# Performance work log

Hardware: AMD Instinct MI355X
Metric: run time of the kernel (lower is better)

Reference implementation:

```python
import jax, jax.numpy as jnp
import numpy as np

B, T, D, E, H, F, K = 4, 2048, 2048, 16, 1024, 1024, 2


def setup_inputs() -> dict:
    key = jax.random.key(0)
    ks = jax.random.split(key, 7)
    sD, sH, sF = D ** -0.5, H ** -0.5, F ** -0.5
    hidden_state = jax.random.normal(ks[0], (B, T, D), jnp.float32)
    Wr = jax.random.normal(ks[1], (D, E), jnp.float32) * sD      # router
    Wg = jax.random.normal(ks[2], (D, 1), jnp.float32) * sD      # shared gate
    W1 = jax.random.normal(ks[3], (E, D, H), jnp.float32) * sD   # expert up-proj
    W2 = jax.random.normal(ks[4], (E, H, D), jnp.float32) * sH   # expert down-proj
    W1s = jax.random.normal(ks[5], (D, F), jnp.float32) * sD     # shared expert up
    W2s = jax.random.normal(ks[6], (F, D), jnp.float32) * sF     # shared expert down
    return {"hidden_state": hidden_state, "Wr": Wr, "Wg": Wg,
            "W1": W1, "W2": W2, "W1s": W1s, "W2s": W2s}


def reference(hidden_state, Wr, Wg, W1, W2, W1s, W2s):
    b, t, d = hidden_state.shape
    N = b * t
    x = hidden_state.reshape(N, d)

    # Router: softmax scores + shared-expert sigmoid gate
    s = jax.nn.softmax(x @ Wr, axis=-1)           # [N, E]
    g_shared = jax.nn.sigmoid(x @ Wg)             # [N, 1]

    topk_vals, topk_idx = jax.lax.top_k(s, K)     # [N, K]

    # Dense combine weights: gate[n,e] = topk_vals if expert e chosen, else 0.
    # Mathematically identical to sort/gather/scatter-add dispatch in the source.
    gate = jnp.zeros((N, E), dtype=s.dtype).at[
        jnp.arange(N)[:, None], topk_idx].add(topk_vals)

    # Per-expert FFN (fixed small expert loop), gate-weighted combine
    y = jnp.zeros_like(x)
    for e in range(E):
        h = jax.nn.gelu(x @ W1[e], approximate=False)   # [N, H]
        y = y + gate[:, e:e + 1] * (h @ W2[e])

    # Shared expert, scaled by sigmoid gate
    shared = jax.nn.gelu(x @ W1s, approximate=False) @ W2s
    y = y + g_shared * shared
    y_out = y.reshape(b, t, d)

    # Aux stats (attention_mask is None branch)
    importance = s.mean(axis=0)                               # [E]
    counts = jnp.zeros((E,), jnp.float32).at[topk_idx.reshape(-1)].add(1.0)
    load = counts / (counts.sum() + 1e-12)
    return y_out, importance, load
```

## Files before the change

### kernel.cpp

```cpp
#include <hip/hip_runtime.h>
#include <hip/hip_bf16.h>


#define N_TOK 8192
#define DDIM  2048
#define NEXP  16
#define HDIM  1024
#define FDIM  1024
#define NASSIGN (N_TOK * 2)
#define NROWS (NASSIGN + N_TOK)

typedef __attribute__((ext_vector_type(8))) short bf16x8;
typedef __attribute__((ext_vector_type(4))) float f32x4;
typedef __attribute__((ext_vector_type(8))) unsigned short u16x8;
typedef __attribute__((ext_vector_type(4))) unsigned short u16x4;

__device__ inline unsigned short f2bf(float f) {
    unsigned int u = __builtin_bit_cast(unsigned int, f);
    u += 0x7FFFu + ((u >> 16) & 1u);
    return (unsigned short)(u >> 16);
}

__device__ inline float bf2f(unsigned short h) {
    return __builtin_bit_cast(float, (unsigned int)h << 16);
}

__device__ inline float gelu_f(float v) {
    return 0.5f * v * (1.0f + erff(v * 0.7071067811865475f));
}

__device__ inline void gld16(void* lds, const void* g) {
    __builtin_amdgcn_global_load_lds(
        (const __attribute__((address_space(1))) unsigned int*)g,
        (__attribute__((address_space(3))) unsigned int*)lds, 16, 0, 0);
}

__global__ __launch_bounds__(256) void zero_small(float* imp) {
    if (threadIdx.x < NEXP) imp[threadIdx.x] = 0.0f;
}

__global__ __launch_bounds__(256) void cast_x_kernel(const float* __restrict__ x,
                                                     unsigned short* __restrict__ xb) {
    size_t i = (size_t)blockIdx.x * 256 + threadIdx.x;
    const float4 a = ((const float4*)x)[i * 2];
    const float4 b = ((const float4*)x)[i * 2 + 1];
    u16x8 o;
    o[0] = f2bf(a.x); o[1] = f2bf(a.y); o[2] = f2bf(a.z); o[3] = f2bf(a.w);
    o[4] = f2bf(b.x); o[5] = f2bf(b.y); o[6] = f2bf(b.z); o[7] = f2bf(b.w);
    *(u16x8*)(xb + i * 8) = o;
}

template <int R, int C>
__global__ __launch_bounds__(256) void transpose_cast(const float* __restrict__ src,
                                                      unsigned short* __restrict__ dst) {
    __shared__ unsigned short t[64][66];
    const size_t zoff = (size_t)blockIdx.z * R * C;
    src += zoff; dst += zoff;
    const int r0 = blockIdx.y * 64, c0 = blockIdx.x * 64;
    const int tid = threadIdx.x;
    const int cr = tid >> 4;
    const int cc4 = (tid & 15) * 4;
#pragma unroll
    for (int it = 0; it < 4; ++it) {
        int row = cr + it * 16;
        const float4 v = *(const float4*)(src + (size_t)(r0 + row) * C + c0 + cc4);
        t[row][cc4 + 0] = f2bf(v.x); t[row][cc4 + 1] = f2bf(v.y);
        t[row][cc4 + 2] = f2bf(v.z); t[row][cc4 + 3] = f2bf(v.w);
    }
    __syncthreads();
#pragma unroll
    for (int it = 0; it < 4; ++it) {
        int cc = cr + it * 16;
        u16x4 o;
#pragma unroll
        for (int j = 0; j < 4; ++j) o[j] = t[cc4 + j][cc];
        *(u16x4*)(dst + (size_t)(c0 + cc) * R + r0 + cc4) = o;
    }
}

__global__ __launch_bounds__(256) void router_kernel(
    const float* __restrict__ x, const float* __restrict__ Wr, const float* __restrict__ Wg,
    float* __restrict__ gsh, int* __restrict__ t2i, float* __restrict__ t2v,
    float* __restrict__ imp) {
    __shared__ float simp[NEXP];
    const int tid = threadIdx.x, lane = tid & 63, w = tid >> 6;
    if (tid < NEXP) simp[tid] = 0.0f;
    __syncthreads();
    const int n = blockIdx.x * 4 + w;
    const float* xr = x + (size_t)n * DDIM;
    float acc[NEXP];
#pragma unroll
    for (int e = 0; e < NEXP; ++e) acc[e] = 0.0f;
    float ag = 0.0f;
    for (int j = 0; j < DDIM / 64; ++j) {
        int d = lane + j * 64;
        float xv = xr[d];
        const float* wr = Wr + (size_t)d * NEXP;
#pragma unroll
        for (int e = 0; e < NEXP; ++e) acc[e] = fmaf(xv, wr[e], acc[e]);
        ag = fmaf(xv, Wg[d], ag);
    }
#pragma unroll
    for (int off = 32; off; off >>= 1) {
#pragma unroll
        for (int e = 0; e < NEXP; ++e) acc[e] += __shfl_xor(acc[e], off);
        ag += __shfl_xor(ag, off);
    }
    if (lane == 0) {
        float mx = acc[0];
#pragma unroll
        for (int e = 1; e < NEXP; ++e) mx = fmaxf(mx, acc[e]);
        float p[NEXP], s = 0.0f;
#pragma unroll
        for (int e = 0; e < NEXP; ++e) { p[e] = expf(acc[e] - mx); s += p[e]; }
        const float inv = 1.0f / s;
        int i1 = 0; float v1 = -1.0f;
#pragma unroll
        for (int e = 0; e < NEXP; ++e) {
            p[e] *= inv;
            if (p[e] > v1) { v1 = p[e]; i1 = e; }
        }
        int i2 = 0; float v2 = -1.0f;
#pragma unroll
        for (int e = 0; e < NEXP; ++e) {
            if (e != i1 && p[e] > v2) { v2 = p[e]; i2 = e; }
        }
        t2i[2 * n] = i1; t2i[2 * n + 1] = i2;
        t2v[2 * n] = v1; t2v[2 * n + 1] = v2;
        gsh[n] = 1.0f / (1.0f + expf(-ag));
#pragma unroll
        for (int e = 0; e < NEXP; ++e) atomicAdd(&simp[e], p[e]);
    }
    __syncthreads();
    if (tid < NEXP) unsafeAtomicAdd(&imp[tid], simp[tid]);
}

__global__ __launch_bounds__(256) void scan_finalize(
    const int* __restrict__ t2i, const float* __restrict__ imp,
    int* __restrict__ offs, int* __restrict__ fill, float* __restrict__ out_tail) {
    __shared__ int hist[NEXP];
    const int tid = threadIdx.x;
    if (tid < NEXP) hist[tid] = 0;
    __syncthreads();
    for (int i = tid; i < NASSIGN; i += 256) atomicAdd(&hist[t2i[i]], 1);
    __syncthreads();
    if (tid == 0) {
        int o = 0;
        for (int e = 0; e < NEXP; ++e) { offs[e] = o; o += hist[e]; }
        offs[NEXP] = o;
        offs[NEXP + 1] = NROWS;
    }
    if (tid < NEXP) {
        fill[tid] = 0;
        out_tail[tid] = imp[tid] * (1.0f / (float)N_TOK);
        out_tail[NEXP + tid] = (float)hist[tid] / (float)NASSIGN;
    }
}

__global__ __launch_bounds__(256) void build_assign(
    const int* __restrict__ t2i, const float* __restrict__ t2v,
    const int* __restrict__ offs, int* __restrict__ fill,
    const float* __restrict__ gsh,
    int* __restrict__ atok, float* __restrict__ agate, int* __restrict__ t2pos) {
    const int n = blockIdx.x * 256 + threadIdx.x;
#pragma unroll
    for (int k = 0; k < 2; ++k) {
        int e = t2i[2 * n + k];
        int pos = offs[e] + atomicAdd(&fill[e], 1);
        atok[pos] = n;
        agate[pos] = t2v[2 * n + k];
        t2pos[2 * n + k] = pos;
    }
    atok[NASSIGN + n] = n;
    agate[NASSIGN + n] = gsh[n];
}

__global__ __launch_bounds__(256) void combine_kernel(
    const unsigned short* __restrict__ contrib, const int* __restrict__ t2pos,
    float* __restrict__ y) {
    const int gi = blockIdx.x * 256 + threadIdx.x;
    const int n = gi >> 8;
    const int d8 = (gi & 255) * 8;
    const int p0 = t2pos[2 * n], p1 = t2pos[2 * n + 1];
    u16x8 a = *(const u16x8*)(contrib + (size_t)p0 * DDIM + d8);
    u16x8 b = *(const u16x8*)(contrib + (size_t)p1 * DDIM + d8);
    u16x8 c = *(const u16x8*)(contrib + (size_t)(NASSIGN + n) * DDIM + d8);
    float4 y0, y1;
    y0.x = bf2f(a[0]) + bf2f(b[0]) + bf2f(c[0]);
    y0.y = bf2f(a[1]) + bf2f(b[1]) + bf2f(c[1]);
    y0.z = bf2f(a[2]) + bf2f(b[2]) + bf2f(c[2]);
    y0.w = bf2f(a[3]) + bf2f(b[3]) + bf2f(c[3]);
    y1.x = bf2f(a[4]) + bf2f(b[4]) + bf2f(c[4]);
    y1.y = bf2f(a[5]) + bf2f(b[5]) + bf2f(c[5]);
    y1.z = bf2f(a[6]) + bf2f(b[6]) + bf2f(c[6]);
    y1.w = bf2f(a[7]) + bf2f(b[7]) + bf2f(c[7]);
    float* yr = y + (size_t)n * DDIM + d8;
    *(float4*)yr = y0;
    *(float4*)(yr + 4) = y1;
}

template <int MODE>
__global__ __launch_bounds__(256, 4) void gemm128(
    const unsigned short* __restrict__ A, const unsigned short* __restrict__ B,
    unsigned short* __restrict__ out,
    const int* __restrict__ offs, const int* __restrict__ atok,
    const float* __restrict__ agate) {
    constexpr int KD = MODE == 0 ? DDIM : HDIM;
    constexpr int NC = MODE == 0 ? HDIM : DDIM;
    const int e = blockIdx.z;
    const int m0 = offs[e];
    const int mE = offs[e + 1] - m0;
    const int tm = blockIdx.y;
    if (tm * 128 >= mE) return;
    const int n0 = blockIdx.x * 128;

    __shared__ __align__(16) unsigned short As_[2][128 * 32];
    __shared__ __align__(16) unsigned short Bs_[2][128 * 32];

    const int tid = threadIdx.x, lane = tid & 63;
    const int wid = tid >> 6, wm = wid >> 1, wn = wid & 1;

    const unsigned short* sA[2];
    const unsigned short* sB[2];
    int dOff[2];
#pragma unroll
    for (int it = 0; it < 2; ++it) {
        int c = tid + it * 256;
        int row = c >> 2, slot = c & 3;
        int ksw = (slot ^ ((row >> 1) & 3)) * 8;
        int arow = tm * 128 + row; arow = arow < mE ? arow : mE - 1;
        if (MODE == 0)
            sA[it] = A + (size_t)atok[m0 + arow] * KD + ksw;
        else
            sA[it] = A + (size_t)(m0 + arow) * KD + ksw;
        sB[it] = B + (size_t)e * KD * NC + (size_t)(n0 + row) * KD + ksw;
        dOff[it] = c * 16;
    }

    f32x4 acc[4][4] = {};

    auto stage = [&](int b, int kk) {
        gld16((char*)As_[b] + dOff[0], sA[0] + kk);
        gld16((char*)As_[b] + dOff[1], sA[1] + kk);
        gld16((char*)Bs_[b] + dOff[0], sB[0] + kk);
        gld16((char*)Bs_[b] + dOff[1], sB[1] + kk);
    };
    auto compute = [&](int b) {
        const int c16 = lane & 15, q = lane >> 4;
        bf16x8 av[4], bv[4];
#pragma unroll
        for (int mi = 0; mi < 4; ++mi) {
            int r = wm * 64 + mi * 16 + c16;
            int s = q ^ ((r >> 1) & 3);
            av[mi] = *(const bf16x8*)((const char*)As_[b] + r * 64 + s * 16);
        }
#pragma unroll
        for (int ni = 0; ni < 4; ++ni) {
            int r = wn * 64 + ni * 16 + c16;
            int s = q ^ ((r >> 1) & 3);
            bv[ni] = *(const bf16x8*)((const char*)Bs_[b] + r * 64 + s * 16);
        }
#pragma unroll
        for (int mi = 0; mi < 4; ++mi)
#pragma unroll
            for (int ni = 0; ni < 4; ++ni)
                acc[mi][ni] = __builtin_amdgcn_mfma_f32_16x16x32_bf16(
                    av[mi], bv[ni], acc[mi][ni], 0, 0, 0);
    };

    stage(0, 0);
    __syncthreads();

#pragma unroll 1
    for (int kk = 0; kk < KD; kk += 64) {
        stage(1, kk + 32);
        compute(0);
        __syncthreads();
        if (kk + 64 < KD) stage(0, kk + 64);
        compute(1);
        __syncthreads();
    }

    const int col = lane & 15, r4 = (lane >> 4) * 4;
#pragma unroll
    for (int mi = 0; mi < 4; ++mi) {
#pragma unroll
        for (int r = 0; r < 4; ++r) {
            int grow = tm * 128 + wm * 64 + mi * 16 + r4 + r;
            if (grow >= mE) continue;
            float gate = (MODE == 0) ? agate[m0 + grow] : 0.0f;
#pragma unroll
            for (int ni = 0; ni < 4; ++ni) {
                int gcol = n0 + wn * 64 + ni * 16 + col;
                float v = acc[mi][ni][r];
                if (MODE == 0)
                    out[(size_t)(m0 + grow) * NC + gcol] = f2bf(gelu_f(v) * gate);
                else
                    out[(size_t)(m0 + grow) * NC + gcol] = f2bf(v);
            }
        }
    }
}

extern "C" void kernel_launch(void* const* d_in, const int* in_sizes, int n_in,
                              void* d_out, int out_size, void* d_ws, size_t ws_size,
                              hipStream_t stream) {
    const float* x   = (const float*)d_in[0];
    const float* Wr  = (const float*)d_in[1];
    const float* Wg  = (const float*)d_in[2];
    const float* W1  = (const float*)d_in[3];
    const float* W2  = (const float*)d_in[4];
    const float* W1s = (const float*)d_in[5];
    const float* W2s = (const float*)d_in[6];
    float* out = (float*)d_out;

    char* ws = (char*)d_ws;
    size_t off = 0;
    auto carve = [&](size_t bytes) { char* p = ws + off; off += (bytes + 255) & ~(size_t)255; return p; };
    unsigned short* xb    = (unsigned short*)carve((size_t)N_TOK * DDIM * 2);
    unsigned short* w1all = (unsigned short*)carve((size_t)(NEXP + 1) * DDIM * HDIM * 2);
    unsigned short* w2all = (unsigned short*)carve((size_t)(NEXP + 1) * HDIM * DDIM * 2);
    unsigned short* hb    = (unsigned short*)carve((size_t)NROWS * HDIM * 2);
    float* gsh            = (float*)carve((size_t)N_TOK * 4);
    int* t2i              = (int*)carve((size_t)N_TOK * 2 * 4);
    float* t2v            = (float*)carve((size_t)N_TOK * 2 * 4);
    int* atok             = (int*)carve((size_t)NROWS * 4);
    float* agate          = (float*)carve((size_t)NROWS * 4);
    int* t2pos            = (int*)carve((size_t)NASSIGN * 4);
    float* imp            = (float*)carve(256);
    int* offs             = (int*)carve(256);
    int* fill             = (int*)carve(256);
    if (ws_size < off) return;

    unsigned short* contrib = (unsigned short*)ws;

    float* out_tail = out + (size_t)N_TOK * DDIM;

    hipLaunchKernelGGL(zero_small, dim3(1), dim3(256), 0, stream, imp);
    hipLaunchKernelGGL(cast_x_kernel, dim3(N_TOK * DDIM / 8 / 256), dim3(256), 0, stream, x, xb);
    hipLaunchKernelGGL((transpose_cast<DDIM, HDIM>), dim3(HDIM / 64, DDIM / 64, NEXP), dim3(256), 0, stream, W1, w1all);
    hipLaunchKernelGGL((transpose_cast<DDIM, HDIM>), dim3(HDIM / 64, DDIM / 64, 1), dim3(256), 0, stream,
                       W1s, w1all + (size_t)NEXP * DDIM * HDIM);
    hipLaunchKernelGGL((transpose_cast<HDIM, DDIM>), dim3(DDIM / 64, HDIM / 64, NEXP), dim3(256), 0, stream, W2, w2all);
    hipLaunchKernelGGL((transpose_cast<HDIM, DDIM>), dim3(DDIM / 64, HDIM / 64, 1), dim3(256), 0, stream,
                       W2s, w2all + (size_t)NEXP * HDIM * DDIM);
    hipLaunchKernelGGL(router_kernel, dim3(N_TOK / 4), dim3(256), 0, stream, x, Wr, Wg, gsh, t2i, t2v, imp);
    hipLaunchKernelGGL(scan_finalize, dim3(1), dim3(256), 0, stream, t2i, imp, offs, fill, out_tail);
    hipLaunchKernelGGL(build_assign, dim3(N_TOK / 256), dim3(256), 0, stream, t2i, t2v, offs, fill, gsh, atok, agate, t2pos);

    hipLaunchKernelGGL((gemm128<0>), dim3(HDIM / 128, N_TOK / 128, NEXP + 1), dim3(256), 0, stream,
                       xb, w1all, hb, offs, atok, agate);
    hipLaunchKernelGGL((gemm128<1>), dim3(DDIM / 128, N_TOK / 128, NEXP + 1), dim3(256), 0, stream,
                       hb, w2all, contrib, offs, atok, agate);
    hipLaunchKernelGGL(combine_kernel, dim3(N_TOK * DDIM / 8 / 256), dim3(256), 0, stream,
                       contrib, t2pos, out);
}
```

Before: 614.6 us.

## Fuse bf16 cast of x into router and swizzle grouped GEMM block order

The standalone cast_x kernel is removed and the bf16 conversion of x is written from the router kernel, which already reads x. This saves one full pass over the fp32 activations and one launch. The grouped GEMMs now use a flattened 1D grid with an XCD-style modulo-8 remap of block indices to 3D coordinates, so that blocks sharing tiles land on the same chiplet L2. The router's bf16 stores are 2-byte strided per lane, so they coalesce less well than the old vectorized cast.

```diff
diff --git a/kernel.cpp b/kernel.cpp
--- a/kernel.cpp
+++ b/kernel.cpp
@@ -37,17 +37,6 @@
 
 __global__ __launch_bounds__(256) void zero_small(float* imp) {
     if (threadIdx.x < NEXP) imp[threadIdx.x] = 0.0f;
-}
-
-__global__ __launch_bounds__(256) void cast_x_kernel(const float* __restrict__ x,
-                                                     unsigned short* __restrict__ xb) {
-    size_t i = (size_t)blockIdx.x * 256 + threadIdx.x;
-    const float4 a = ((const float4*)x)[i * 2];
-    const float4 b = ((const float4*)x)[i * 2 + 1];
-    u16x8 o;
-    o[0] = f2bf(a.x); o[1] = f2bf(a.y); o[2] = f2bf(a.z); o[3] = f2bf(a.w);
-    o[4] = f2bf(b.x); o[5] = f2bf(b.y); o[6] = f2bf(b.z); o[7] = f2bf(b.w);
-    *(u16x8*)(xb + i * 8) = o;
 }
 
 template <int R, int C>
@@ -80,6 +69,7 @@
 
 __global__ __launch_bounds__(256) void router_kernel(
     const float* __restrict__ x, const float* __restrict__ Wr, const float* __restrict__ Wg,
+    unsigned short* __restrict__ xb,
     float* __restrict__ gsh, int* __restrict__ t2i, float* __restrict__ t2v,
     float* __restrict__ imp) {
     __shared__ float simp[NEXP];
@@ -88,6 +78,7 @@
     __syncthreads();
     const int n = blockIdx.x * 4 + w;
     const float* xr = x + (size_t)n * DDIM;
+    unsigned short* xbr = xb + (size_t)n * DDIM;
     float acc[NEXP];
 #pragma unroll
     for (int e = 0; e < NEXP; ++e) acc[e] = 0.0f;
@@ -95,6 +86,7 @@
     for (int j = 0; j < DDIM / 64; ++j) {
         int d = lane + j * 64;
         float xv = xr[d];
+        xbr[d] = f2bf(xv);
         const float* wr = Wr + (size_t)d * NEXP;
 #pragma unroll
         for (int e = 0; e < NEXP; ++e) acc[e] = fmaf(xv, wr[e], acc[e]);
@@ -207,12 +199,22 @@
     const float* __restrict__ agate) {
     constexpr int KD = MODE == 0 ? DDIM : HDIM;
     constexpr int NC = MODE == 0 ? HDIM : DDIM;
-    const int e = blockIdx.z;
+    constexpr int NX = NC / 128;
+    constexpr int NY = N_TOK / 128;
+    constexpr int NZ = NEXP + 1;
+    constexpr int NB = NX * NY * NZ;
+    static_assert(NB % 8 == 0, "bijective swizzle needs NB % 8 == 0");
+
+    const int L = blockIdx.x;
+    const int orig = (L & 7) * (NB / 8) + (L >> 3);
+    const int bx = orig % NX;
+    const int tm = (orig / NX) % NY;
+    const int e  = orig / (NX * NY);
+
     const int m0 = offs[e];
     const int mE = offs[e + 1] - m0;
-    const int tm = blockIdx.y;
     if (tm * 128 >= mE) return;
-    const int n0 = blockIdx.x * 128;
+    const int n0 = bx * 128;
 
     __shared__ __align__(16) unsigned short As_[2][128 * 32];
     __shared__ __align__(16) unsigned short Bs_[2][128 * 32];
@@ -337,20 +339,19 @@
     float* out_tail = out + (size_t)N_TOK * DDIM;
 
     hipLaunchKernelGGL(zero_small, dim3(1), dim3(256), 0, stream, imp);
-    hipLaunchKernelGGL(cast_x_kernel, dim3(N_TOK * DDIM / 8 / 256), dim3(256), 0, stream, x, xb);
     hipLaunchKernelGGL((transpose_cast<DDIM, HDIM>), dim3(HDIM / 64, DDIM / 64, NEXP), dim3(256), 0, stream, W1, w1all);
     hipLaunchKernelGGL((transpose_cast<DDIM, HDIM>), dim3(HDIM / 64, DDIM / 64, 1), dim3(256), 0, stream,
                        W1s, w1all + (size_t)NEXP * DDIM * HDIM);
     hipLaunchKernelGGL((transpose_cast<HDIM, DDIM>), dim3(DDIM / 64, HDIM / 64, NEXP), dim3(256), 0, stream, W2, w2all);
     hipLaunchKernelGGL((transpose_cast<HDIM, DDIM>), dim3(DDIM / 64, HDIM / 64, 1), dim3(256), 0, stream,
                        W2s, w2all + (size_t)NEXP * HDIM * DDIM);
-    hipLaunchKernelGGL(router_kernel, dim3(N_TOK / 4), dim3(256), 0, stream, x, Wr, Wg, gsh, t2i, t2v, imp);
+    hipLaunchKernelGGL(router_kernel, dim3(N_TOK / 4), dim3(256), 0, stream, x, Wr, Wg, xb, gsh, t2i, t2v, imp);
     hipLaunchKernelGGL(scan_finalize, dim3(1), dim3(256), 0, stream, t2i, imp, offs, fill, out_tail);
     hipLaunchKernelGGL(build_assign, dim3(N_TOK / 256), dim3(256), 0, stream, t2i, t2v, offs, fill, gsh, atok, agate, t2pos);
 
-    hipLaunchKernelGGL((gemm128<0>), dim3(HDIM / 128, N_TOK / 128, NEXP + 1), dim3(256), 0, stream,
+    hipLaunchKernelGGL((gemm128<0>), dim3((HDIM / 128) * (N_TOK / 128) * (NEXP + 1)), dim3(256), 0, stream,
                        xb, w1all, hb, offs, atok, agate);
-    hipLaunchKernelGGL((gemm128<1>), dim3(DDIM / 128, N_TOK / 128, NEXP + 1), dim3(256), 0, stream,
+    hipLaunchKernelGGL((gemm128<1>), dim3((DDIM / 128) * (N_TOK / 128) * (NEXP + 1)), dim3(256), 0, stream,
                        hb, w2all, contrib, offs, atok, agate);
     hipLaunchKernelGGL(combine_kernel, dim3(N_TOK * DDIM / 8 / 256), dim3(256), 0, stream,
                        contrib, t2pos, out);
```

Result: slower. 966.5 us (+57.2%).

## Triple-buffer GEMM LDS pipeline and fuse x bf16 cast into router

Applied to the files above, without the earlier changes.

The grouped GEMM moves from a double-buffered K loop with two __syncthreads per 64-wide step to a three-stage LDS ring. Each tile step now needs one barrier, and explicit vmcnt waits keep a prefetch in flight while computing. Separately, the standalone x→bf16 cast kernel is removed and the router writes xb as it reads x, saving one full pass over x and a launch. The extra LDS buffer lowers the occupancy bound from 4 to 3 blocks per SM, and the router's 2-byte per-lane stores are narrow.

```diff
diff --git a/kernel.cpp b/kernel.cpp
--- a/kernel.cpp
+++ b/kernel.cpp
@@ -37,17 +37,6 @@
 
 __global__ __launch_bounds__(256) void zero_small(float* imp) {
     if (threadIdx.x < NEXP) imp[threadIdx.x] = 0.0f;
-}
-
-__global__ __launch_bounds__(256) void cast_x_kernel(const float* __restrict__ x,
-                                                     unsigned short* __restrict__ xb) {
-    size_t i = (size_t)blockIdx.x * 256 + threadIdx.x;
-    const float4 a = ((const float4*)x)[i * 2];
-    const float4 b = ((const float4*)x)[i * 2 + 1];
-    u16x8 o;
-    o[0] = f2bf(a.x); o[1] = f2bf(a.y); o[2] = f2bf(a.z); o[3] = f2bf(a.w);
-    o[4] = f2bf(b.x); o[5] = f2bf(b.y); o[6] = f2bf(b.z); o[7] = f2bf(b.w);
-    *(u16x8*)(xb + i * 8) = o;
 }
 
 template <int R, int C>
@@ -80,6 +69,7 @@
 
 __global__ __launch_bounds__(256) void router_kernel(
     const float* __restrict__ x, const float* __restrict__ Wr, const float* __restrict__ Wg,
+    unsigned short* __restrict__ xb,
     float* __restrict__ gsh, int* __restrict__ t2i, float* __restrict__ t2v,
     float* __restrict__ imp) {
     __shared__ float simp[NEXP];
@@ -88,6 +78,7 @@
     __syncthreads();
     const int n = blockIdx.x * 4 + w;
     const float* xr = x + (size_t)n * DDIM;
+    unsigned short* xbr = xb + (size_t)n * DDIM;
     float acc[NEXP];
 #pragma unroll
     for (int e = 0; e < NEXP; ++e) acc[e] = 0.0f;
@@ -95,6 +86,7 @@
     for (int j = 0; j < DDIM / 64; ++j) {
         int d = lane + j * 64;
         float xv = xr[d];
+        xbr[d] = f2bf(xv);
         const float* wr = Wr + (size_t)d * NEXP;
 #pragma unroll
         for (int e = 0; e < NEXP; ++e) acc[e] = fmaf(xv, wr[e], acc[e]);
@@ -200,13 +192,14 @@
 }
 
 template <int MODE>
-__global__ __launch_bounds__(256, 4) void gemm128(
+__global__ __launch_bounds__(256, 3) void gemm128(
     const unsigned short* __restrict__ A, const unsigned short* __restrict__ B,
     unsigned short* __restrict__ out,
     const int* __restrict__ offs, const int* __restrict__ atok,
     const float* __restrict__ agate) {
     constexpr int KD = MODE == 0 ? DDIM : HDIM;
     constexpr int NC = MODE == 0 ? HDIM : DDIM;
+    constexpr int NT = KD / 32;
     const int e = blockIdx.z;
     const int m0 = offs[e];
     const int mE = offs[e + 1] - m0;
@@ -214,8 +207,8 @@
     if (tm * 128 >= mE) return;
     const int n0 = blockIdx.x * 128;
 
-    __shared__ __align__(16) unsigned short As_[2][128 * 32];
-    __shared__ __align__(16) unsigned short Bs_[2][128 * 32];
+    __shared__ __align__(16) unsigned short As_[3][128 * 32];
+    __shared__ __align__(16) unsigned short Bs_[3][128 * 32];
 
     const int tid = threadIdx.x, lane = tid & 63;
     const int wid = tid >> 6, wm = wid >> 1, wn = wid & 1;
@@ -239,7 +232,8 @@
 
     f32x4 acc[4][4] = {};
 
-    auto stage = [&](int b, int kk) {
+    auto stage = [&](int b, int t) {
+        const int kk = t * 32;
         gld16((char*)As_[b] + dOff[0], sA[0] + kk);
         gld16((char*)As_[b] + dOff[1], sA[1] + kk);
         gld16((char*)Bs_[b] + dOff[0], sB[0] + kk);
@@ -269,16 +263,33 @@
     };
 
     stage(0, 0);
-    __syncthreads();
-
+    stage(1, 1);
+    asm volatile("s_waitcnt vmcnt(4)" ::: "memory");
+    __builtin_amdgcn_sched_barrier(0);
+    __builtin_amdgcn_s_barrier();
+    __builtin_amdgcn_sched_barrier(0);
+
+    int b = 0, bn = 2;
 #pragma unroll 1
-    for (int kk = 0; kk < KD; kk += 64) {
-        stage(1, kk + 32);
-        compute(0);
-        __syncthreads();
-        if (kk + 64 < KD) stage(0, kk + 64);
-        compute(1);
-        __syncthreads();
+    for (int t = 0; t < NT; ++t) {
+        if (t + 2 < NT) {
+            stage(bn, t + 2);
+            compute(b);
+            asm volatile("s_waitcnt vmcnt(4)" ::: "memory");
+            __builtin_amdgcn_sched_barrier(0);
+            __builtin_amdgcn_s_barrier();
+            __builtin_amdgcn_sched_barrier(0);
+        } else if (t + 1 < NT) {
+            compute(b);
+            asm volatile("s_waitcnt vmcnt(0)" ::: "memory");
+            __builtin_amdgcn_sched_barrier(0);
+            __builtin_amdgcn_s_barrier();
+            __builtin_amdgcn_sched_barrier(0);
+        } else {
+            compute(b);
+        }
+        b = (b == 2) ? 0 : b + 1;
+        bn = (bn == 2) ? 0 : bn + 1;
     }
 
     const int col = lane & 15, r4 = (lane >> 4) * 4;
@@ -337,14 +348,13 @@
     float* out_tail = out + (size_t)N_TOK * DDIM;
 
     hipLaunchKernelGGL(zero_small, dim3(1), dim3(256), 0, stream, imp);
-    hipLaunchKernelGGL(cast_x_kernel, dim3(N_TOK * DDIM / 8 / 256), dim3(256), 0, stream, x, xb);
     hipLaunchKernelGGL((transpose_cast<DDIM, HDIM>), dim3(HDIM / 64, DDIM / 64, NEXP), dim3(256), 0, stream, W1, w1all);
     hipLaunchKernelGGL((transpose_cast<DDIM, HDIM>), dim3(HDIM / 64, DDIM / 64, 1), dim3(256), 0, stream,
                        W1s, w1all + (size_t)NEXP * DDIM * HDIM);
     hipLaunchKernelGGL((transpose_cast<HDIM, DDIM>), dim3(DDIM / 64, HDIM / 64, NEXP), dim3(256), 0, stream, W2, w2all);
     hipLaunchKernelGGL((transpose_cast<HDIM, DDIM>), dim3(DDIM / 64, HDIM / 64, 1), dim3(256), 0, stream,
                        W2s, w2all + (size_t)NEXP * HDIM * DDIM);
-    hipLaunchKernelGGL(router_kernel, dim3(N_TOK / 4), dim3(256), 0, stream, x, Wr, Wg, gsh, t2i, t2v, imp);
+    hipLaunchKernelGGL(router_kernel, dim3(N_TOK / 4), dim3(256), 0, stream, x, Wr, Wg, xb, gsh, t2i, t2v, imp);
     hipLaunchKernelGGL(scan_finalize, dim3(1), dim3(256), 0, stream, t2i, imp, offs, fill, out_tail);
     hipLaunchKernelGGL(build_assign, dim3(N_TOK / 256), dim3(256), 0, stream, t2i, t2v, offs, fill, gsh, atok, agate, t2pos);
 
```

After: 813.1 us. 32.3% more time.
